# Optimization experiments

Measured on AMD Instinct MI355X. Metric: run time of the kernel, lower is better.

Reference implementation:

```python
import jax, jax.numpy as jnp
import numpy as np
from jax import lax

D_MODEL, D_STATE, D_CONV, EXPAND = 512, 16, 4, 2
D_INNER = EXPAND * D_MODEL          # 1024
DT_RANK = (D_MODEL + 15) // 16      # 32
BATCH, SEQ = 4, 1024


def setup_inputs() -> dict:
    key = jax.random.key(0)
    ks = jax.random.split(key, 8)
    s = 0.02
    x = jax.random.normal(ks[0], (BATCH, SEQ, D_MODEL), jnp.float32)
    in_proj_w = jax.random.normal(ks[1], (2 * D_INNER, D_MODEL), jnp.float32) * s
    conv_w = jax.random.normal(ks[2], (D_INNER, 1, D_CONV), jnp.float32) * s  # depthwise
    conv_b = jnp.zeros((D_INNER,), jnp.float32)
    x_proj_w = jax.random.normal(ks[3], (DT_RANK + 2 * D_STATE, D_INNER), jnp.float32) * s
    dt_proj_w = jax.random.normal(ks[4], (D_INNER, DT_RANK), jnp.float32) * s
    dt_proj_b = jax.random.normal(ks[5], (D_INNER,), jnp.float32) * 0.1
    # Mamba S4D-real init: A = -[1..d_state] per channel, stored as log
    A_log = jnp.log(jnp.tile(jnp.arange(1, D_STATE + 1, dtype=jnp.float32)[None, :], (D_INNER, 1)))
    D = jnp.ones((D_INNER,), jnp.float32)
    out_proj_w = jax.random.normal(ks[6], (D_MODEL, D_INNER), jnp.float32) * s
    ln_w = jnp.ones((D_MODEL,), jnp.float32)
    ln_b = jnp.zeros((D_MODEL,), jnp.float32)
    return dict(x=x, in_proj_w=in_proj_w, conv_w=conv_w, conv_b=conv_b,
                x_proj_w=x_proj_w, dt_proj_w=dt_proj_w, dt_proj_b=dt_proj_b,
                A_log=A_log, D=D, out_proj_w=out_proj_w, ln_w=ln_w, ln_b=ln_b)


def _selective_scan(u, delta, A, Bm, Cm, D):
    # u, delta: (B,L,Di); A: (Di,N); Bm, Cm: (B,L,N)
    dA = jnp.exp(delta[..., None] * A)                    # (B,L,Di,N)
    dBu = (delta * u)[..., None] * Bm[:, :, None, :]      # (B,L,Di,N)
    dA_t = jnp.moveaxis(dA, 1, 0)                         # (L,B,Di,N)
    dBu_t = jnp.moveaxis(dBu, 1, 0)
    C_t = jnp.moveaxis(Cm, 1, 0)                          # (L,B,N)

    def step(h, inp):
        dA_i, dBu_i, C_i = inp
        h = dA_i * h + dBu_i                              # (B,Di,N)
        y = jnp.einsum('bdn,bn->bd', h, C_i)
        return h, y

    h0 = jnp.zeros((u.shape[0], A.shape[0], A.shape[1]), u.dtype)
    _, ys = lax.scan(step, h0, (dA_t, dBu_t, C_t))        # ys: (L,B,Di)
    return jnp.moveaxis(ys, 0, 1) + u * D                 # (B,L,Di)


def reference(x, in_proj_w, conv_w, conv_b, x_proj_w, dt_proj_w, dt_proj_b,
              A_log, D, out_proj_w, ln_w, ln_b):
    # ---- Mamba SSM ----
    xz = jnp.einsum('bld,ed->ble', x, in_proj_w)          # (B,L,2*Di)
    xs, z = jnp.split(xz, 2, axis=-1)
    # causal depthwise conv over time
    xt = jnp.moveaxis(xs, 1, 2)                           # (B,Di,L)
    xt = lax.conv_general_dilated(xt, conv_w, window_strides=(1,),
                                  padding=[(D_CONV - 1, 0)],
                                  feature_group_count=D_INNER,
                                  dimension_numbers=('NCH', 'OIH', 'NCH'))
    xt = xt + conv_b[None, :, None]
    u = jax.nn.silu(jnp.moveaxis(xt, 1, 2))               # (B,L,Di)

    x_dbl = jnp.einsum('bld,ed->ble', u, x_proj_w)        # (B,L,dt_rank+2N)
    dt = x_dbl[..., :DT_RANK]
    Bm = x_dbl[..., DT_RANK:DT_RANK + D_STATE]
    Cm = x_dbl[..., DT_RANK + D_STATE:]
    delta = jax.nn.softplus(jnp.einsum('blr,dr->bld', dt, dt_proj_w) + dt_proj_b)
    A = -jnp.exp(A_log)                                   # (Di,N)

    y = _selective_scan(u, delta, A, Bm, Cm, D)
    y = y * jax.nn.silu(z)
    ssm_out = jnp.einsum('ble,de->bld', y, out_proj_w)    # (B,L,Dm)

    # ---- residual + LayerNorm ----
    r = x + ssm_out
    mu = jnp.mean(r, axis=-1, keepdims=True)
    var = jnp.mean(jnp.square(r - mu), axis=-1, keepdims=True)
    return (r - mu) / jnp.sqrt(var + 1e-5) * ln_w + ln_b
```

## Files before the change

### kernel.cpp

```cpp
#include <hip/hip_runtime.h>
#include <hip/hip_bf16.h>
#include <math.h>

#define B_   4
#define L_   1024
#define DM   512
#define DI   1024
#define NS   16
#define XDC  64
#define BL   4096
#define KS   4
#define CL   256

typedef short bfrag __attribute__((ext_vector_type(8)));
typedef float ffrag __attribute__((ext_vector_type(4)));

__device__ __forceinline__ ushort f2bf(float v) {
    __hip_bfloat16 h = __float2bfloat16(v);
    return *(ushort*)&h;
}

template<bool F32>
__device__ __forceinline__ void stage8(const void* p, size_t eoff, ushort* dst) {
    if constexpr (F32) {
        const float* f = (const float*)p + eoff;
        float4 v0 = *(const float4*)f;
        float4 v1 = *(const float4*)(f + 4);
        *(ushort4*)dst       = make_ushort4(f2bf(v0.x), f2bf(v0.y), f2bf(v0.z), f2bf(v0.w));
        *(ushort4*)(dst + 4) = make_ushort4(f2bf(v1.x), f2bf(v1.y), f2bf(v1.z), f2bf(v1.w));
    } else {
        *(uint4*)dst = *(const uint4*)((const ushort*)p + eoff);
    }
}

template<int EPI, bool AF, bool BF>
__global__ __launch_bounds__(256) void gemm_mfma(const void* __restrict__ Ap,
        const void* __restrict__ Bp, float* __restrict__ C,
        int K, int ldc, const float* __restrict__ resid)
{
    __shared__ ushort As[128][40];
    __shared__ ushort Bs[128][40];
    const int tid = threadIdx.x;
    const int lane = tid & 63, wave = tid >> 6;
    const int wm = (wave & 1) * 64, wn = (wave >> 1) * 64;
    const int l15 = lane & 15, quad = lane >> 4;
    const int m0 = blockIdx.y * 128, n0 = blockIdx.x * 128;

    ffrag acc[4][4] = {};

    for (int k0 = 0; k0 < K; k0 += 32) {
        #pragma unroll
        for (int i = 0; i < 2; i++) {
            int chunk = tid + i * 256;
            int row = chunk >> 2, kk8 = (chunk & 3) * 8;
            stage8<AF>(Ap, (size_t)(m0 + row) * K + k0 + kk8, &As[row][kk8]);
            stage8<BF>(Bp, (size_t)(n0 + row) * K + k0 + kk8, &Bs[row][kk8]);
        }
        __syncthreads();
        bfrag af[4], bfv[4];
        #pragma unroll
        for (int i = 0; i < 4; i++) {
            af[i]  = *(const bfrag*)&As[wm + i * 16 + l15][quad * 8];
            bfv[i] = *(const bfrag*)&Bs[wn + i * 16 + l15][quad * 8];
        }
        #pragma unroll
        for (int i = 0; i < 4; i++)
            #pragma unroll
            for (int j = 0; j < 4; j++)
                acc[i][j] = __builtin_amdgcn_mfma_f32_16x16x32_bf16(af[i], bfv[j], acc[i][j], 0, 0, 0);
        __syncthreads();
    }

    #pragma unroll
    for (int i = 0; i < 4; i++) {
        #pragma unroll
        for (int j = 0; j < 4; j++) {
            int n = n0 + wn + j * 16 + l15;
            #pragma unroll
            for (int r = 0; r < 4; r++) {
                int m = m0 + wm + i * 16 + quad * 4 + r;
                float v = acc[i][j][r];
                if (EPI == 2) v += resid[(size_t)m * ldc + n];
                C[(size_t)m * ldc + n] = v;
            }
        }
    }
}

__global__ __launch_bounds__(256) void gemm3_splitk(const float* __restrict__ uT,
        const float* __restrict__ xw, float* __restrict__ part)
{
    __shared__ float As[16][33];
    __shared__ float Ws[16][68];
    const int tid = threadIdx.x;
    const int nn = tid & 63;
    const int mg = tid >> 6;
    const int ks = blockIdx.x, m0 = blockIdx.y * 32;
    const int kbase = ks * (DI / KS);
    float acc[8] = {};

    for (int k0 = 0; k0 < DI / KS; k0 += 16) {
        if (tid < 128) {
            int k = tid >> 3, m4 = (tid & 7) * 4;
            const float4 v = *(const float4*)&uT[(size_t)(kbase + k0 + k) * BL + m0 + m4];
            As[k][m4 + 0] = v.x; As[k][m4 + 1] = v.y;
            As[k][m4 + 2] = v.z; As[k][m4 + 3] = v.w;
        }
        {
            int r = tid >> 2, c4 = (tid & 3) * 4;
            const float4 v = *(const float4*)&xw[(size_t)r * DI + kbase + k0 + c4];
            Ws[c4 + 0][r] = v.x; Ws[c4 + 1][r] = v.y;
            Ws[c4 + 2][r] = v.z; Ws[c4 + 3][r] = v.w;
        }
        __syncthreads();
        #pragma unroll
        for (int kk = 0; kk < 16; kk++) {
            float w = Ws[kk][nn];
            #pragma unroll
            for (int i = 0; i < 8; i++)
                acc[i] = fmaf(As[kk][mg * 8 + i], w, acc[i]);
        }
        __syncthreads();
    }

    float* pp = part + (size_t)ks * 64 * BL + (size_t)nn * BL + m0 + mg * 8;
    *(float4*)&pp[0] = make_float4(acc[0], acc[1], acc[2], acc[3]);
    *(float4*)&pp[4] = make_float4(acc[4], acc[5], acc[6], acc[7]);
}

__global__ __launch_bounds__(256) void gemm3_reduce(const float* __restrict__ part,
        float* __restrict__ xdblT)
{
    int i = blockIdx.x * 256 + threadIdx.x;
    const float4* p0 = (const float4*)part;
    float4 a = p0[i];
    #pragma unroll
    for (int s = 1; s < KS; s++) {
        float4 b = p0[i + (size_t)s * 64 * BL / 4];
        a.x += b.x; a.y += b.y; a.z += b.z; a.w += b.w;
    }
    ((float4*)xdblT)[i] = a;
}

__global__ __launch_bounds__(256) void dt_softplus(const float* __restrict__ xdblT,
        const float* __restrict__ dtw, const float* __restrict__ bias,
        float* __restrict__ deltaT)
{
    const int tid = threadIdx.x;
    const int lane = tid & 63;
    const int bl = blockIdx.x * 256 + lane * 4;

    int d = blockIdx.y * 4 + (tid >> 6);
    d = __builtin_amdgcn_readfirstlane(d);
    float wreg[32];
    {
        const float4* wp = (const float4*)(dtw + (size_t)d * 32);
        #pragma unroll
        for (int k = 0; k < 8; k++) *(float4*)&wreg[k * 4] = wp[k];
    }
    const float bb = bias[d];

    float4 acc = make_float4(bb, bb, bb, bb);
    #pragma unroll
    for (int k = 0; k < 32; k++) {
        float4 v = *(const float4*)&xdblT[(size_t)k * BL + bl];
        float w = wreg[k];
        acc.x = fmaf(w, v.x, acc.x);
        acc.y = fmaf(w, v.y, acc.y);
        acc.z = fmaf(w, v.z, acc.z);
        acc.w = fmaf(w, v.w, acc.w);
    }
    float4 o;
    o.x = (acc.x > 20.f) ? acc.x : __logf(1.f + __expf(acc.x));
    o.y = (acc.y > 20.f) ? acc.y : __logf(1.f + __expf(acc.y));
    o.z = (acc.z > 20.f) ? acc.z : __logf(1.f + __expf(acc.z));
    o.w = (acc.w > 20.f) ? acc.w : __logf(1.f + __expf(acc.w));
    *(float4*)&deltaT[(size_t)d * BL + bl] = o;
}

__global__ __launch_bounds__(256) void conv_silu(const float* __restrict__ xzT,
        const float* __restrict__ cw, const float* __restrict__ cb,
        float* __restrict__ uT)
{
    int i = blockIdx.x * 256 + threadIdx.x;
    int d  = i >> 10;
    int q  = i & 1023;
    int bl = q * 4;
    int l  = bl & (L_ - 1);
    const float* row = xzT + (size_t)d * BL;
    float4 cur = *(const float4*)&row[bl];
    float4 prev = make_float4(0.f, 0.f, 0.f, 0.f);
    if (l != 0) prev = *(const float4*)&row[bl - 4];
    float v[7] = { prev.y, prev.z, prev.w, cur.x, cur.y, cur.z, cur.w };
    float w0 = cw[d * 4 + 0], w1 = cw[d * 4 + 1], w2 = cw[d * 4 + 2], w3 = cw[d * 4 + 3];
    float bias = cb[d];
    float4 o;
    o.x = bias + w0 * v[0] + w1 * v[1] + w2 * v[2] + w3 * v[3];
    o.y = bias + w0 * v[1] + w1 * v[2] + w2 * v[3] + w3 * v[4];
    o.z = bias + w0 * v[2] + w1 * v[3] + w2 * v[4] + w3 * v[5];
    o.w = bias + w0 * v[3] + w1 * v[4] + w2 * v[5] + w3 * v[6];
    o.x = o.x / (1.f + __expf(-o.x));
    o.y = o.y / (1.f + __expf(-o.y));
    o.z = o.z / (1.f + __expf(-o.z));
    o.w = o.w / (1.f + __expf(-o.w));
    *(float4*)&uT[(size_t)d * BL + bl] = o;
}

__global__ __launch_bounds__(256) void scan_fused(const float* __restrict__ deltaT,
        const float* __restrict__ uT, const float* __restrict__ xdblT,
        const float* __restrict__ xzT, const float* __restrict__ A_log,
        const float* __restrict__ Dp, float* __restrict__ yT)
{
    const int tid = threadIdx.x;
    const int lane = tid & 63;
    const int bd = blockIdx.x * 4 + (tid >> 6);
    const int d = bd & (DI - 1);
    const int b = bd >> 10;

    float Acoef[16];
    {
        const float4* ap = (const float4*)(A_log + d * NS);
        #pragma unroll
        for (int i = 0; i < 4; i++) {
            float4 v = ap[i];
            Acoef[i * 4 + 0] = -__expf(v.x); Acoef[i * 4 + 1] = -__expf(v.y);
            Acoef[i * 4 + 2] = -__expf(v.z); Acoef[i * 4 + 3] = -__expf(v.w);
        }
    }
    const float Dd = Dp[d];

    const size_t row_t = (size_t)d * BL + b * L_;
    const size_t row_z = (size_t)(DI + d) * BL + b * L_;
    const float* xB = xdblT + (size_t)32 * BL + b * L_;
    const float* xC = xdblT + (size_t)48 * BL + b * L_;

    float h[16];
    #pragma unroll
    for (int n = 0; n < 16; n++) h[n] = 0.f;

    for (int c = 0; c < L_ / CL; c++) {
        const int l0 = c * CL + lane * 4;

        float4 dvv = *(const float4*)&deltaT[row_t + l0];
        float4 uvv = *(const float4*)&uT[row_t + l0];
        float dv[4] = { dvv.x, dvv.y, dvv.z, dvv.w };
        float du[4] = { dvv.x * uvv.x, dvv.y * uvv.y, dvv.z * uvv.z, dvv.w * uvv.w };
        float sa = dv[0] + dv[1] + dv[2] + dv[3];

        float a[16], bb[16];
        #pragma unroll
        for (int n = 0; n < 16; n++) {
            a[n] = __expf(sa * Acoef[n]);
            const float4 Bv = *(const float4*)&xB[(size_t)n * BL + l0];
            float acc = du[0] * Bv.x;
            acc = fmaf(__expf(dv[1] * Acoef[n]), acc, du[1] * Bv.y);
            acc = fmaf(__expf(dv[2] * Acoef[n]), acc, du[2] * Bv.z);
            acc = fmaf(__expf(dv[3] * Acoef[n]), acc, du[3] * Bv.w);
            bb[n] = acc;
        }

        #pragma unroll
        for (int off = 1; off < 64; off <<= 1) {
            #pragma unroll
            for (int n = 0; n < 16; n++) {
                float pa = __shfl_up(a[n], off);
                float pb = __shfl_up(bb[n], off);
                if (lane >= off) {
                    bb[n] = fmaf(a[n], pb, bb[n]);
                    a[n] *= pa;
                }
            }
        }

        #pragma unroll
        for (int n = 0; n < 16; n++) {
            float pa = __shfl_up(a[n], 1);
            float pb = __shfl_up(bb[n], 1);
            float ae = (lane == 0) ? 1.f : pa;
            float be = (lane == 0) ? 0.f : pb;
            h[n] = fmaf(ae, h[n], be);
        }

        float s0 = 0.f, s1 = 0.f, s2 = 0.f, s3 = 0.f;
        #pragma unroll
        for (int n = 0; n < 16; n++) {
            const float4 Bv = *(const float4*)&xB[(size_t)n * BL + l0];
            const float4 Cv = *(const float4*)&xC[(size_t)n * BL + l0];
            float hn = h[n];
            hn = fmaf(__expf(dv[0] * Acoef[n]), hn, du[0] * Bv.x);
            s0 = fmaf(hn, Cv.x, s0);
            hn = fmaf(__expf(dv[1] * Acoef[n]), hn, du[1] * Bv.y);
            s1 = fmaf(hn, Cv.y, s1);
            hn = fmaf(__expf(dv[2] * Acoef[n]), hn, du[2] * Bv.z);
            s2 = fmaf(hn, Cv.z, s2);
            hn = fmaf(__expf(dv[3] * Acoef[n]), hn, du[3] * Bv.w);
            s3 = fmaf(hn, Cv.w, s3);
            h[n] = hn;
        }

        #pragma unroll
        for (int n = 0; n < 16; n++) h[n] = __shfl(h[n], 63);

        float4 zv = *(const float4*)&xzT[row_z + l0];
        float4 yv;
        float v0 = s0 + uvv.x * Dd; yv.x = v0 * (zv.x / (1.f + __expf(-zv.x)));
        float v1 = s1 + uvv.y * Dd; yv.y = v1 * (zv.y / (1.f + __expf(-zv.y)));
        float v2 = s2 + uvv.z * Dd; yv.z = v2 * (zv.z / (1.f + __expf(-zv.z)));
        float v3 = s3 + uvv.w * Dd; yv.w = v3 * (zv.w / (1.f + __expf(-zv.w)));
        *(float4*)&yT[row_t + l0] = yv;
    }
}

__global__ __launch_bounds__(256) void transpose_cast(const float* __restrict__ yT,
        ushort* __restrict__ yB)
{
    __shared__ float t[64][65];
    const int bl0 = blockIdx.x * 64, d0 = blockIdx.y * 64;
    const int tid = threadIdx.x;
    #pragma unroll
    for (int i = 0; i < 4; i++) {
        int chunk = tid + i * 256;
        int dr = chunk >> 4, c4 = (chunk & 15) * 4;
        const float4 v = *(const float4*)&yT[(size_t)(d0 + dr) * BL + bl0 + c4];
        t[dr][c4 + 0] = v.x; t[dr][c4 + 1] = v.y;
        t[dr][c4 + 2] = v.z; t[dr][c4 + 3] = v.w;
    }
    __syncthreads();
    #pragma unroll
    for (int i = 0; i < 4; i++) {
        int chunk = tid + i * 256;
        int br = chunk >> 4, dc4 = (chunk & 15) * 4;
        ushort4 o;
        o.x = f2bf(t[dc4 + 0][br]); o.y = f2bf(t[dc4 + 1][br]);
        o.z = f2bf(t[dc4 + 2][br]); o.w = f2bf(t[dc4 + 3][br]);
        *(ushort4*)&yB[(size_t)(bl0 + br) * DI + d0 + dc4] = o;
    }
}

__global__ __launch_bounds__(256) void ln_kernel(const float* __restrict__ r,
        const float* __restrict__ lnw, const float* __restrict__ lnb,
        float* __restrict__ out)
{
    int row = blockIdx.x;
    const float* rr = r + (size_t)row * DM;
    float v0 = rr[threadIdx.x], v1 = rr[threadIdx.x + 256];
    float s = v0 + v1, s2 = v0 * v0 + v1 * v1;
    #pragma unroll
    for (int off = 32; off > 0; off >>= 1) {
        s  += __shfl_down(s, off);
        s2 += __shfl_down(s2, off);
    }
    __shared__ float ls[4], ls2[4];
    __shared__ float mu_s, rstd_s;
    int wid = threadIdx.x >> 6, lane = threadIdx.x & 63;
    if (lane == 0) { ls[wid] = s; ls2[wid] = s2; }
    __syncthreads();
    if (threadIdx.x == 0) {
        float S = ls[0] + ls[1] + ls[2] + ls[3];
        float S2 = ls2[0] + ls2[1] + ls2[2] + ls2[3];
        float mu = S * (1.f / DM);
        float var = S2 * (1.f / DM) - mu * mu;
        mu_s = mu;
        rstd_s = rsqrtf(var + 1e-5f);
    }
    __syncthreads();
    float mu = mu_s, rstd = rstd_s;
    out[(size_t)row * DM + threadIdx.x] =
        (v0 - mu) * rstd * lnw[threadIdx.x] + lnb[threadIdx.x];
    out[(size_t)row * DM + threadIdx.x + 256] =
        (v1 - mu) * rstd * lnw[threadIdx.x + 256] + lnb[threadIdx.x + 256];
}

extern "C" void kernel_launch(void* const* d_in, const int* in_sizes, int n_in,
                              void* d_out, int out_size, void* d_ws, size_t ws_size,
                              hipStream_t stream)
{
    const float* x         = (const float*)d_in[0];
    const float* in_proj_w = (const float*)d_in[1];
    const float* conv_w    = (const float*)d_in[2];
    const float* conv_b    = (const float*)d_in[3];
    const float* x_proj_w  = (const float*)d_in[4];
    const float* dt_proj_w = (const float*)d_in[5];
    const float* dt_proj_b = (const float*)d_in[6];
    const float* A_log     = (const float*)d_in[7];
    const float* Dvec      = (const float*)d_in[8];
    const float* out_proj_w= (const float*)d_in[9];
    const float* ln_w      = (const float*)d_in[10];
    const float* ln_b      = (const float*)d_in[11];
    float* out = (float*)d_out;

    float* ws     = (float*)d_ws;
    float* xzT    = ws;
    float* uT     = xzT    + (size_t)2048 * BL;
    float* xdblT  = uT     + (size_t)DI * BL;
    float* deltaT = xdblT  + (size_t)XDC * BL;
    float* yT     = deltaT + (size_t)DI * BL;
    float* r      = yT     + (size_t)DI * BL;
    float*  xdblp = yT;
    ushort* yB    = (ushort*)deltaT;

    dim3 blk(256);

    gemm_mfma<0, true, true><<<dim3(BL / 128, 2048 / 128), blk, 0, stream>>>(
        in_proj_w, x, xzT, DM, BL, nullptr);

    conv_silu<<<(DI * BL / 4) / 256, blk, 0, stream>>>(xzT, conv_w, conv_b, uT);

    gemm3_splitk<<<dim3(KS, BL / 32), blk, 0, stream>>>(uT, x_proj_w, xdblp);
    gemm3_reduce<<<(64 * BL / 4) / 256, blk, 0, stream>>>(xdblp, xdblT);

    dt_softplus<<<dim3(BL / 256, DI / 4), blk, 0, stream>>>(
        xdblT, dt_proj_w, dt_proj_b, deltaT);

    scan_fused<<<B_ * DI / 4, blk, 0, stream>>>(
        deltaT, uT, xdblT, xzT, A_log, Dvec, yT);

    transpose_cast<<<dim3(BL / 64, DI / 64), blk, 0, stream>>>(yT, yB);

    gemm_mfma<2, false, true><<<dim3(DM / 128, BL / 128), blk, 0, stream>>>(
        yB, out_proj_w, r, DI, DM, x);

    ln_kernel<<<BL, blk, 0, stream>>>(r, ln_w, ln_b, out);
}
```

Before: 278.1 us.

## Scan whole sequence in one pass with 16 timesteps per lane

The selective scan kernel used to walk the sequence in four chunks of 256 steps, each needing its own 6-level wavefront shuffle scan plus a carry broadcast. Now each lane owns 16 consecutive timesteps, so the 64-lane wave covers all 1024 steps with a single shuffle scan and no cross-chunk carry. This removes three quarters of the shuffle work and the serial chunk dependency. The cost is higher register pressure (dv, uv, du, s arrays of 16, plus a, bb, h) and strided per-lane loads that coalesce less well than the previous lane*4 layout.

```diff
diff --git a/kernel.cpp b/kernel.cpp
--- a/kernel.cpp
+++ b/kernel.cpp
@@ -10,7 +10,6 @@
 #define XDC  64
 #define BL   4096
 #define KS   4
-#define CL   256
 
 typedef short bfrag __attribute__((ext_vector_type(8)));
 typedef float ffrag __attribute__((ext_vector_type(4)));
@@ -229,85 +228,104 @@
     }
     const float Dd = Dp[d];
 
-    const size_t row_t = (size_t)d * BL + b * L_;
-    const size_t row_z = (size_t)(DI + d) * BL + b * L_;
-    const float* xB = xdblT + (size_t)32 * BL + b * L_;
-    const float* xC = xdblT + (size_t)48 * BL + b * L_;
+    const size_t row_t = (size_t)d * BL + b * L_ + lane * 16;
+    const size_t row_z = (size_t)(DI + d) * BL + b * L_ + lane * 16;
+    const float* xB = xdblT + (size_t)32 * BL + b * L_ + lane * 16;
+    const float* xC = xdblT + (size_t)48 * BL + b * L_ + lane * 16;
+
+    float dv[16], uv[16];
+    {
+        const float4* dp = (const float4*)(deltaT + row_t);
+        const float4* up = (const float4*)(uT + row_t);
+        #pragma unroll
+        for (int i = 0; i < 4; i++) {
+            *(float4*)&dv[i * 4] = dp[i];
+            *(float4*)&uv[i * 4] = up[i];
+        }
+    }
+    float du[16];
+    float sa = 0.f;
+    #pragma unroll
+    for (int j = 0; j < 16; j++) { du[j] = dv[j] * uv[j]; sa += dv[j]; }
+
+    float a[16], bb[16];
+    #pragma unroll
+    for (int n = 0; n < 16; n++) {
+        a[n] = __expf(sa * Acoef[n]);
+        const float4* bp = (const float4*)(xB + (size_t)n * BL);
+        float acc;
+        #pragma unroll
+        for (int i = 0; i < 4; i++) {
+            float4 Bv = bp[i];
+            if (i == 0) acc = du[0] * Bv.x;
+            else        acc = fmaf(__expf(dv[i * 4] * Acoef[n]), acc, du[i * 4] * Bv.x);
+            acc = fmaf(__expf(dv[i * 4 + 1] * Acoef[n]), acc, du[i * 4 + 1] * Bv.y);
+            acc = fmaf(__expf(dv[i * 4 + 2] * Acoef[n]), acc, du[i * 4 + 2] * Bv.z);
+            acc = fmaf(__expf(dv[i * 4 + 3] * Acoef[n]), acc, du[i * 4 + 3] * Bv.w);
+        }
+        bb[n] = acc;
+    }
+
+    #pragma unroll
+    for (int off = 1; off < 64; off <<= 1) {
+        #pragma unroll
+        for (int n = 0; n < 16; n++) {
+            float pa = __shfl_up(a[n], off);
+            float pb = __shfl_up(bb[n], off);
+            if (lane >= off) {
+                bb[n] = fmaf(a[n], pb, bb[n]);
+                a[n] *= pa;
+            }
+        }
+    }
 
     float h[16];
     #pragma unroll
-    for (int n = 0; n < 16; n++) h[n] = 0.f;
-
-    for (int c = 0; c < L_ / CL; c++) {
-        const int l0 = c * CL + lane * 4;
-
-        float4 dvv = *(const float4*)&deltaT[row_t + l0];
-        float4 uvv = *(const float4*)&uT[row_t + l0];
-        float dv[4] = { dvv.x, dvv.y, dvv.z, dvv.w };
-        float du[4] = { dvv.x * uvv.x, dvv.y * uvv.y, dvv.z * uvv.z, dvv.w * uvv.w };
-        float sa = dv[0] + dv[1] + dv[2] + dv[3];
-
-        float a[16], bb[16];
-        #pragma unroll
-        for (int n = 0; n < 16; n++) {
-            a[n] = __expf(sa * Acoef[n]);
-            const float4 Bv = *(const float4*)&xB[(size_t)n * BL + l0];
-            float acc = du[0] * Bv.x;
-            acc = fmaf(__expf(dv[1] * Acoef[n]), acc, du[1] * Bv.y);
-            acc = fmaf(__expf(dv[2] * Acoef[n]), acc, du[2] * Bv.z);
-            acc = fmaf(__expf(dv[3] * Acoef[n]), acc, du[3] * Bv.w);
-            bb[n] = acc;
-        }
-
-        #pragma unroll
-        for (int off = 1; off < 64; off <<= 1) {
-            #pragma unroll
-            for (int n = 0; n < 16; n++) {
-                float pa = __shfl_up(a[n], off);
-                float pb = __shfl_up(bb[n], off);
-                if (lane >= off) {
-                    bb[n] = fmaf(a[n], pb, bb[n]);
-                    a[n] *= pa;
-                }
-            }
-        }
-
-        #pragma unroll
-        for (int n = 0; n < 16; n++) {
-            float pa = __shfl_up(a[n], 1);
-            float pb = __shfl_up(bb[n], 1);
-            float ae = (lane == 0) ? 1.f : pa;
-            float be = (lane == 0) ? 0.f : pb;
-            h[n] = fmaf(ae, h[n], be);
-        }
-
-        float s0 = 0.f, s1 = 0.f, s2 = 0.f, s3 = 0.f;
-        #pragma unroll
-        for (int n = 0; n < 16; n++) {
-            const float4 Bv = *(const float4*)&xB[(size_t)n * BL + l0];
-            const float4 Cv = *(const float4*)&xC[(size_t)n * BL + l0];
-            float hn = h[n];
-            hn = fmaf(__expf(dv[0] * Acoef[n]), hn, du[0] * Bv.x);
-            s0 = fmaf(hn, Cv.x, s0);
-            hn = fmaf(__expf(dv[1] * Acoef[n]), hn, du[1] * Bv.y);
-            s1 = fmaf(hn, Cv.y, s1);
-            hn = fmaf(__expf(dv[2] * Acoef[n]), hn, du[2] * Bv.z);
-            s2 = fmaf(hn, Cv.z, s2);
-            hn = fmaf(__expf(dv[3] * Acoef[n]), hn, du[3] * Bv.w);
-            s3 = fmaf(hn, Cv.w, s3);
-            h[n] = hn;
-        }
-
-        #pragma unroll
-        for (int n = 0; n < 16; n++) h[n] = __shfl(h[n], 63);
-
-        float4 zv = *(const float4*)&xzT[row_z + l0];
-        float4 yv;
-        float v0 = s0 + uvv.x * Dd; yv.x = v0 * (zv.x / (1.f + __expf(-zv.x)));
-        float v1 = s1 + uvv.y * Dd; yv.y = v1 * (zv.y / (1.f + __expf(-zv.y)));
-        float v2 = s2 + uvv.z * Dd; yv.z = v2 * (zv.z / (1.f + __expf(-zv.z)));
-        float v3 = s3 + uvv.w * Dd; yv.w = v3 * (zv.w / (1.f + __expf(-zv.w)));
-        *(float4*)&yT[row_t + l0] = yv;
+    for (int n = 0; n < 16; n++) {
+        float pb = __shfl_up(bb[n], 1);
+        h[n] = (lane == 0) ? 0.f : pb;
+    }
+
+    float s[16];
+    #pragma unroll
+    for (int j = 0; j < 16; j++) s[j] = 0.f;
+    #pragma unroll
+    for (int n = 0; n < 16; n++) {
+        const float4* bp = (const float4*)(xB + (size_t)n * BL);
+        const float4* cp = (const float4*)(xC + (size_t)n * BL);
+        float hn = h[n];
+        #pragma unroll
+        for (int i = 0; i < 4; i++) {
+            float4 Bv = bp[i];
+            float4 Cv = cp[i];
+            hn = fmaf(__expf(dv[i * 4 + 0] * Acoef[n]), hn, du[i * 4 + 0] * Bv.x);
+            s[i * 4 + 0] = fmaf(hn, Cv.x, s[i * 4 + 0]);
+            hn = fmaf(__expf(dv[i * 4 + 1] * Acoef[n]), hn, du[i * 4 + 1] * Bv.y);
+            s[i * 4 + 1] = fmaf(hn, Cv.y, s[i * 4 + 1]);
+            hn = fmaf(__expf(dv[i * 4 + 2] * Acoef[n]), hn, du[i * 4 + 2] * Bv.z);
+            s[i * 4 + 2] = fmaf(hn, Cv.z, s[i * 4 + 2]);
+            hn = fmaf(__expf(dv[i * 4 + 3] * Acoef[n]), hn, du[i * 4 + 3] * Bv.w);
+            s[i * 4 + 3] = fmaf(hn, Cv.w, s[i * 4 + 3]);
+        }
+    }
+
+    {
+        const float4* zp = (const float4*)(xzT + row_z);
+        float4* yp = (float4*)(yT + row_t);
+        #pragma unroll
+        for (int i = 0; i < 4; i++) {
+            float4 zv = zp[i];
+            float4 yv;
+            float v0 = s[i * 4 + 0] + uv[i * 4 + 0] * Dd;
+            float v1 = s[i * 4 + 1] + uv[i * 4 + 1] * Dd;
+            float v2 = s[i * 4 + 2] + uv[i * 4 + 2] * Dd;
+            float v3 = s[i * 4 + 3] + uv[i * 4 + 3] * Dd;
+            yv.x = v0 * (zv.x / (1.f + __expf(-zv.x)));
+            yv.y = v1 * (zv.y / (1.f + __expf(-zv.y)));
+            yv.z = v2 * (zv.z / (1.f + __expf(-zv.z)));
+            yv.w = v3 * (zv.w / (1.f + __expf(-zv.w)));
+            yp[i] = yv;
+        }
     }
 }
 
```

Result: faster. 266.3 us, median of 2 (-4.2%).
